# Kernel tuning notes

Measured on AMD Instinct MI355X. Metric: run time of the kernel, lower is better.

The kernel has to match this reference:

```python
import jax, jax.numpy as jnp
import numpy as np

N = 50000      # total nodes
E = 500000     # edges
D = 128        # in_channels
B = 50         # graphs in batch
NPG = N // B   # nodes per graph (equal-sized graphs)
RATIO = 0.5
ALPHA = 0.6


def setup_inputs() -> dict:
    key = jax.random.key(0)
    ks = jax.random.split(key, 8)
    x = jax.random.normal(ks[0], (N, D), dtype=jnp.float32)
    edge_index = jax.random.randint(ks[1], (2, E), 0, N, dtype=jnp.int32)
    batch = jnp.repeat(jnp.arange(B, dtype=jnp.int32), NPG)  # sorted, equal blocks
    s = 1.0 / np.sqrt(D)
    # GCNConv(D,1) for structure score
    W_s = jax.random.normal(ks[2], (D, 1), dtype=jnp.float32) * s
    b_s = jnp.zeros((1,), dtype=jnp.float32)
    # Linear(D,1) for feature score
    W_f = jax.random.normal(ks[3], (1, D), dtype=jnp.float32) * s
    b_f = jnp.zeros((1,), dtype=jnp.float32)
    # GCNConv(D,D) fusion layer
    W_fu = jax.random.normal(ks[4], (D, D), dtype=jnp.float32) * s
    b_fu = jnp.zeros((D,), dtype=jnp.float32)
    return {"x": x, "edge_index": edge_index, "batch": batch,
            "W_s": W_s, "b_s": b_s, "W_f": W_f, "b_f": b_f,
            "W_fu": W_fu, "b_fu": b_fu}


def gcn_conv(x, src, dst, W, b, n):
    """PyG GCNConv: add self loops, symmetric D^-1/2 (A+I) D^-1/2 @ (xW) + b."""
    xw = x @ W                                  # [n, out]
    loop = jnp.arange(n, dtype=src.dtype)
    s = jnp.concatenate([src, loop])
    d = jnp.concatenate([dst, loop])
    deg = jax.ops.segment_sum(jnp.ones_like(s, dtype=xw.dtype), d, num_segments=n)
    dinv = jax.lax.rsqrt(jnp.maximum(deg, 1e-12))
    norm = dinv[s] * dinv[d]                    # [E+n]
    out = jax.ops.segment_sum(norm[:, None] * xw[s], d, num_segments=n)
    return out + b


def reference(x, edge_index, batch, W_s, b_s, W_f, b_f, W_fu, b_fu):
    src, dst = edge_index[0], edge_index[1]
    # fused score: alpha * structure (GCN) + (1-alpha) * feature (Linear)
    score_s = gcn_conv(x, src, dst, W_s, b_s, N)[:, 0]          # [N]
    score_f = (x @ W_f.T + b_f)[:, 0]                           # [N]
    score = jnp.tanh(ALPHA * score_s + (1.0 - ALPHA) * score_f)
    # per-graph top-k (equal-sized graphs -> dense [B, NPG] view, like the torch topk)
    k = int(np.ceil(RATIO * NPG))
    dense = score.reshape(B, NPG)
    order = jnp.argsort(-dense, axis=-1)                        # descending
    offsets = (jnp.arange(B, dtype=jnp.int32) * NPG)[:, None]
    perm = (order[:, :k].astype(jnp.int32) + offsets).reshape(-1)  # [B*k]
    # fusion conv on full graph, then gather selected nodes
    x_fused = gcn_conv(x, src, dst, W_fu, b_fu, N)              # [N, D]
    x_ae = x_fused[perm]                                        # [B*k, D]
    x_out = x_ae * score[perm][:, None]                         # multiplier == 1
    batch_out = batch[perm]
    # filter_adj: remap node ids, keep edges with both endpoints selected
    nodemap = jnp.full((N,), -1, dtype=jnp.int32).at[perm].set(
        jnp.arange(perm.shape[0], dtype=jnp.int32))
    r, c = nodemap[src], nodemap[dst]
    m = (r >= 0) & (c >= 0)
    edge_index_new = jnp.stack([r[m], c[m]], axis=0)
    return (x_out, edge_index_new, batch_out, perm, x_ae)
```

## Files before the change

kernel.cpp:

```cpp
#include <hip/hip_runtime.h>
#include <math.h>

#define N_NODES 50000
#define N_EDGES 500000
#define DIM     128
#define NGRAPH  50
#define NPGC    1000
#define KSEL    500
#define SORT_N  1024
#define NBE     489
#define NBN     49
#define GEMM_BLKS 782
#define DEG_BLKS  1954
#define DOTS_BLKS 12500
#define NDINV     196
#define GATH_BLKS 6250

typedef short s16x8 __attribute__((ext_vector_type(8)));
typedef float f32x4 __attribute__((ext_vector_type(4)));

__device__ __forceinline__ void f2bf2(float v, unsigned short& h, unsigned short& l) {
    unsigned u = __float_as_uint(v);
    unsigned hb = (u + 0x7FFFu + ((u >> 16) & 1u)) >> 16;
    h = (unsigned short)hb;
    float r = v - __uint_as_float(hb << 16);
    unsigned u2 = __float_as_uint(r);
    l = (unsigned short)((u2 + 0x7FFFu + ((u2 >> 16) & 1u)) >> 16);
}


__global__ __launch_bounds__(256) void k0_wprep(const float* __restrict__ W,
                                                unsigned short* __restrict__ Wth,
                                                unsigned short* __restrict__ Wtl) {
    int idx = blockIdx.x * 256 + threadIdx.x;
    int k = idx >> 7, ch = idx & 127;
    unsigned short h, l;
    f2bf2(W[idx], h, l);
    int hh = k >> 6, kl = k & 63;
    int pos = hh * 8192 + ch * 64 + ((((kl >> 3) ^ (ch & 7))) << 3) + (kl & 7);
    Wth[pos] = h;
    Wtl[pos] = l;
}


__global__ __launch_bounds__(256) void k1_gemm_deg(const float* __restrict__ x,
                                                   const unsigned short* __restrict__ Wth,
                                                   const unsigned short* __restrict__ Wtl,
                                                   float* __restrict__ xw,
                                                   const int* __restrict__ dst,
                                                   int* __restrict__ deg) {
    __shared__ unsigned short lds_sh[24576];
    int t = threadIdx.x;
    if (blockIdx.x >= GEMM_BLKS) {
        int e = (blockIdx.x - GEMM_BLKS) * 256 + t;
        if (e < N_EDGES) atomicAdd(&deg[dst[e]], 1);
        return;
    }
    unsigned short* XH = lds_sh;
    unsigned short* XL = lds_sh + 4096;
    unsigned short* WH = lds_sh + 8192;
    unsigned short* WL = lds_sh + 16384;
    const int wv = t >> 6, lane = t & 63;
    const int q = lane >> 4, mm = lane & 15;
    int node_base = blockIdx.x * 64;

    f32x4 zero4v = {0.f, 0.f, 0.f, 0.f};
    f32x4 acc[8];
    #pragma unroll
    for (int ct = 0; ct < 8; ct++) acc[ct] = zero4v;

    for (int h = 0; h < 2; h++) {
        {
            const s16x8* GH = (const s16x8*)(Wth + h * 8192);
            const s16x8* GL = (const s16x8*)(Wtl + h * 8192);
            s16x8* LH = (s16x8*)WH;
            s16x8* LL = (s16x8*)WL;
            #pragma unroll
            for (int i = 0; i < 4; i++) {
                LH[t + i * 256] = GH[t + i * 256];
                LL[t + i * 256] = GL[t + i * 256];
            }
        }
        #pragma unroll
        for (int i = 0; i < 4; i++) {
            int f = t + i * 256;
            int r = f >> 4, c4 = f & 15;
            int node = node_base + r;
            float4 v = make_float4(0.f, 0.f, 0.f, 0.f);
            if (node < N_NODES) v = *(const float4*)&x[(size_t)node * DIM + h * 64 + c4 * 4];
            unsigned short h0, l0, h1, l1, h2, l2, h3, l3;
            f2bf2(v.x, h0, l0); f2bf2(v.y, h1, l1);
            f2bf2(v.z, h2, l2); f2bf2(v.w, h3, l3);
            int off = r * 64 + ((((c4 >> 1) ^ (r & 7))) << 3) + ((c4 & 1) << 2);
            *(uint2*)&XH[off] = make_uint2((unsigned)h0 | ((unsigned)h1 << 16),
                                           (unsigned)h2 | ((unsigned)h3 << 16));
            *(uint2*)&XL[off] = make_uint2((unsigned)l0 | ((unsigned)l1 << 16),
                                           (unsigned)l2 | ((unsigned)l3 << 16));
        }
        __syncthreads();
        #pragma unroll
        for (int c = 0; c < 2; c++) {
            int jb = c * 4 + q;
            int aoff = (wv * 16 + mm) * 64 + ((jb ^ (mm & 7)) << 3);
            s16x8 ah = *(const s16x8*)&XH[aoff];
            s16x8 al = *(const s16x8*)&XL[aoff];
            #pragma unroll
            for (int ct = 0; ct < 8; ct++) {
                int ch = ct * 16 + mm;
                int boff = ch * 64 + ((jb ^ (ch & 7)) << 3);
                s16x8 bh = *(const s16x8*)&WH[boff];
                s16x8 bl = *(const s16x8*)&WL[boff];
                acc[ct] = __builtin_amdgcn_mfma_f32_16x16x32_bf16(ah, bh, acc[ct], 0, 0, 0);
                acc[ct] = __builtin_amdgcn_mfma_f32_16x16x32_bf16(ah, bl, acc[ct], 0, 0, 0);
                acc[ct] = __builtin_amdgcn_mfma_f32_16x16x32_bf16(al, bh, acc[ct], 0, 0, 0);
            }
        }
        __syncthreads();
    }
    #pragma unroll
    for (int ct = 0; ct < 8; ct++) {
        #pragma unroll
        for (int r = 0; r < 4; r++) {
            int node = node_base + wv * 16 + q * 4 + r;
            if (node < N_NODES) xw[(size_t)node * DIM + ct * 16 + mm] = acc[ct][r];
        }
    }
}


__global__ __launch_bounds__(256) void k2_dots_scan_dinv(const int* __restrict__ deg,
                                                         int* __restrict__ rowoff,
                                                         int* __restrict__ bsumsN,
                                                         const float* __restrict__ x,
                                                         const float* __restrict__ Ws,
                                                         const float* __restrict__ Wf,
                                                         const float* __restrict__ bf,
                                                         double* __restrict__ pack,
                                                         float* __restrict__ dinvf,
                                                         double* __restrict__ sf) {
    int t = threadIdx.x;
    int lane = t & 63, wid = t >> 6;
    int bid = blockIdx.x;
    if (bid < DOTS_BLKS) {
        int node = bid * 4 + wid;
        const float* xr = x + (size_t)node * DIM;
        double x1 = (double)xr[lane], x2 = (double)xr[lane + 64];
        double ps = x1 * (double)Ws[lane] + x2 * (double)Ws[lane + 64];
        double pf = x1 * (double)Wf[lane] + x2 * (double)Wf[lane + 64];
        for (int off = 32; off > 0; off >>= 1) {
            ps += __shfl_down(ps, off, 64);
            pf += __shfl_down(pf, off, 64);
        }
        if (lane == 0) {
            pack[2 * node + 1] = ps;
            sf[node] = pf + (double)bf[0];
        }
        return;
    }
    if (bid < DOTS_BLKS + NBN) {
        __shared__ int ws4[4];
        int base = (bid - DOTS_BLKS) * 1024 + t * 4;
        int v0 = (base + 0 < N_NODES) ? deg[base + 0] : 0;
        int v1 = (base + 1 < N_NODES) ? deg[base + 1] : 0;
        int v2 = (base + 2 < N_NODES) ? deg[base + 2] : 0;
        int v3 = (base + 3 < N_NODES) ? deg[base + 3] : 0;
        int s4 = v0 + v1 + v2 + v3;
        int incl = s4;
        #pragma unroll
        for (int off = 1; off < 64; off <<= 1) {
            int u = __shfl_up(incl, off, 64);
            if (lane >= off) incl += u;
        }
        if (lane == 63) ws4[wid] = incl;
        __syncthreads();
        int woff = 0;
        #pragma unroll
        for (int w = 0; w < 4; w++) if (w < wid) woff += ws4[w];
        int excl = incl - s4 + woff;
        if (base + 0 < N_NODES) rowoff[base + 0] = excl;
        if (base + 1 < N_NODES) rowoff[base + 1] = excl + v0;
        if (base + 2 < N_NODES) rowoff[base + 2] = excl + v0 + v1;
        if (base + 3 < N_NODES) rowoff[base + 3] = excl + v0 + v1 + v2;
        if (t == 255) bsumsN[bid - DOTS_BLKS] = woff + incl;
        return;
    }
    int i = (bid - DOTS_BLKS - NBN) * 256 + t;
    if (i < N_NODES) {
        double di = 1.0 / sqrt((double)(deg[i] + 1));
        pack[2 * i] = di;
        dinvf[i] = (float)di;
    }
}


__global__ __launch_bounds__(256) void k3_csr(const int* __restrict__ src,
                                              const int* __restrict__ dst,
                                              const int* __restrict__ rowoff,
                                              const int* __restrict__ bsumsN,
                                              int* __restrict__ cursor,
                                              int* __restrict__ csr) {
    __shared__ int bsN[64];
    int t = threadIdx.x;
    if (t < 64) {
        int v = (t < NBN) ? bsumsN[t] : 0;
        int incl = v;
        #pragma unroll
        for (int off = 1; off < 64; off <<= 1) {
            int u = __shfl_up(incl, off, 64);
            if (t >= off) incl += u;
        }
        bsN[t] = incl - v;
    }
    __syncthreads();
    int e = blockIdx.x * 256 + t;
    if (e >= N_EDGES) return;
    int d = dst[e];
    int pos = rowoff[d] + bsN[d >> 10] + atomicAdd(&cursor[d], 1);
    csr[pos] = src[e];
}


__global__ __launch_bounds__(1024) void k4_topk(const int* __restrict__ csr,
                                                const int* __restrict__ rowoff,
                                                const int* __restrict__ bsumsN,
                                                const int* __restrict__ deg,
                                                const double* __restrict__ pack,
                                                const double* __restrict__ sf,
                                                const float* __restrict__ bs,
                                                int* __restrict__ perm, int* __restrict__ nodemap,
                                                float* __restrict__ scoref_sel,
                                                float* __restrict__ out, long o2, long o3) {
    __shared__ double key[SORT_N];
    __shared__ int    idx[SORT_N];
    __shared__ int    bsN[64];
    int g = blockIdx.x, t = threadIdx.x;
    if (t < 64) {
        int v = (t < NBN) ? bsumsN[t] : 0;
        int incl = v;
        #pragma unroll
        for (int off = 1; off < 64; off <<= 1) {
            int u = __shfl_up(incl, off, 64);
            if (t >= off) incl += u;
        }
        bsN[t] = incl - v;
    }
    __syncthreads();
    const double A = 0.6, OMA = 1.0 - 0.6;
    double bsv = (double)bs[0];
    {
        int i = t;
        if (i < NPGC) {
            int node = g * NPGC + i;
            int base = rowoff[node] + bsN[node >> 10];
            int cnt  = deg[node];
            double acc0 = 0.0, acc1 = 0.0;
            int e = 0;
            for (; e + 2 <= cnt; e += 2) {
                int s0 = csr[base + e];
                int s1 = csr[base + e + 1];
                double2 p0 = ((const double2*)pack)[s0];
                double2 p1 = ((const double2*)pack)[s1];
                acc0 += p0.x * p0.y;
                acc1 += p1.x * p1.y;
            }
            if (e < cnt) {
                int s0 = csr[base + e];
                double2 p0 = ((const double2*)pack)[s0];
                acc0 += p0.x * p0.y;
            }
            double2 pn = ((const double2*)pack)[node];
            double tot = pn.x * (acc0 + acc1) + pn.x * pn.x * pn.y + bsv;
            key[i] = tanh(A * tot + OMA * sf[node]);
            idx[i] = i;
        } else if (i < SORT_N) { key[i] = -1e300; idx[i] = i; }
    }
    __syncthreads();
    for (int size = 2; size <= SORT_N; size <<= 1) {
        for (int stride = size >> 1; stride > 0; stride >>= 1) {
            if (t < 512) {
                int a = ((t & ~(stride - 1)) << 1) | (t & (stride - 1));
                int b = a | stride;
                bool descFirst = ((a & size) == 0);
                double ka = key[a], kb = key[b];
                int ia = idx[a], ib = idx[b];
                bool aAfterB = (ka < kb) || (ka == kb && ia > ib);
                if (descFirst ? aAfterB : !aAfterB) {
                    key[a] = kb; key[b] = ka;
                    idx[a] = ib; idx[b] = ia;
                }
            }
            __syncthreads();
        }
    }
    if (t < KSEL) {
        int j = t;
        int node = g * NPGC + idx[j];
        int pos  = g * KSEL + j;
        perm[pos]        = node;
        nodemap[node]    = pos + 1;
        scoref_sel[pos]  = (float)key[j];
        out[o2 + pos]    = (float)g;
        out[o3 + pos]    = (float)node;
    }
}


__global__ __launch_bounds__(256) void k5_escan_gather(const int* __restrict__ src,
                                                       const int* __restrict__ dst,
                                                       const int* __restrict__ nodemap,
                                                       int* __restrict__ epos,
                                                       int* __restrict__ bsumsE,
                                                       const float* __restrict__ xw,
                                                       const int* __restrict__ perm,
                                                       const int* __restrict__ rowoff,
                                                       const int* __restrict__ bsumsN,
                                                       const int* __restrict__ deg,
                                                       const int* __restrict__ csr,
                                                       const float* __restrict__ dinvf,
                                                       const float* __restrict__ scoref_sel,
                                                       const float* __restrict__ b_fu,
                                                       float* __restrict__ out, long o4) {
    int t = threadIdx.x;
    int lane = t & 63, wid = t >> 6;
    if (blockIdx.x < NBE) {
        __shared__ int ws4[4];
        int base = blockIdx.x * 1024 + t * 4;
        int v0 = 0, v1 = 0, v2 = 0, v3 = 0;
        if (base + 0 < N_EDGES) v0 = (nodemap[src[base + 0]] > 0 && nodemap[dst[base + 0]] > 0);
        if (base + 1 < N_EDGES) v1 = (nodemap[src[base + 1]] > 0 && nodemap[dst[base + 1]] > 0);
        if (base + 2 < N_EDGES) v2 = (nodemap[src[base + 2]] > 0 && nodemap[dst[base + 2]] > 0);
        if (base + 3 < N_EDGES) v3 = (nodemap[src[base + 3]] > 0 && nodemap[dst[base + 3]] > 0);
        int s4 = v0 + v1 + v2 + v3;
        int incl = s4;
        #pragma unroll
        for (int off = 1; off < 64; off <<= 1) {
            int u = __shfl_up(incl, off, 64);
            if (lane >= off) incl += u;
        }
        if (lane == 63) ws4[wid] = incl;
        __syncthreads();
        int woff = 0;
        #pragma unroll
        for (int w = 0; w < 4; w++) if (w < wid) woff += ws4[w];
        int excl = incl - s4 + woff;
        if (base + 0 < N_EDGES) epos[base + 0] = excl;
        if (base + 1 < N_EDGES) epos[base + 1] = excl + v0;
        if (base + 2 < N_EDGES) epos[base + 2] = excl + v0 + v1;
        if (base + 3 < N_EDGES) epos[base + 3] = excl + v0 + v1 + v2;
        if (t == 255) bsumsE[blockIdx.x] = woff + incl;
        return;
    }
    __shared__ int bsN[64];
    if (t < 64) {
        int v = (t < NBN) ? bsumsN[t] : 0;
        int incl = v;
        #pragma unroll
        for (int off = 1; off < 64; off <<= 1) {
            int u = __shfl_up(incl, off, 64);
            if (t >= off) incl += u;
        }
        bsN[t] = incl - v;
    }
    __syncthreads();
    int wave = (blockIdx.x - NBE) * 4 + wid;
    int p = perm[wave];
    float dpf = dinvf[p];
    int c2 = lane * 2;
    float2 v = ((const float2*)(xw + (size_t)p * DIM))[lane];
    float nself = dpf * dpf;
    float ax = nself * v.x, ay = nself * v.y;
    int beg = rowoff[p] + bsN[p >> 10], cnt = deg[p];
    int i = 0;
    for (; i + 2 <= cnt; i += 2) {
        int s0 = csr[beg + i];
        int s1 = csr[beg + i + 1];
        float2 u0 = ((const float2*)(xw + (size_t)s0 * DIM))[lane];
        float2 u1 = ((const float2*)(xw + (size_t)s1 * DIM))[lane];
        float n0 = dinvf[s0] * dpf, n1 = dinvf[s1] * dpf;
        ax += n0 * u0.x; ay += n0 * u0.y;
        ax += n1 * u1.x; ay += n1 * u1.y;
    }
    if (i < cnt) {
        int s0 = csr[beg + i];
        float2 u0 = ((const float2*)(xw + (size_t)s0 * DIM))[lane];
        float n0 = dinvf[s0] * dpf;
        ax += n0 * u0.x; ay += n0 * u0.y;
    }
    ax += b_fu[c2];
    ay += b_fu[c2 + 1];
    float sc = scoref_sel[wave];
    size_t ro = (size_t)wave * DIM + c2;
    out[o4 + ro]     = ax;
    out[o4 + ro + 1] = ay;
    out[ro]          = ax * sc;
    out[ro + 1]      = ay * sc;
}


__global__ __launch_bounds__(256) void k6_compact(const int* __restrict__ src,
                                                  const int* __restrict__ dst,
                                                  const int* __restrict__ nodemap,
                                                  const int* __restrict__ epos,
                                                  const int* __restrict__ bsumsE,
                                                  float* __restrict__ out_edges, long M) {
    __shared__ int bsE[512];
    int t = threadIdx.x;
    if (t < 64) {
        int carry = 0;
        #pragma unroll
        for (int c = 0; c < 8; c++) {
            int i = c * 64 + t;
            int v = (i < NBE) ? bsumsE[i] : 0;
            int incl = v;
            #pragma unroll
            for (int off = 1; off < 64; off <<= 1) {
                int u = __shfl_up(incl, off, 64);
                if (t >= off) incl += u;
            }
            if (i < 512) bsE[i] = incl - v + carry;
            carry += __shfl(incl, 63, 64);
        }
    }
    __syncthreads();
    int e = blockIdx.x * 256 + t;
    if (e >= N_EDGES) return;
    int r = nodemap[src[e]], c = nodemap[dst[e]];
    if (r > 0 && c > 0) {
        int pos = epos[e] + bsE[e >> 10];
        out_edges[pos]     = (float)(r - 1);
        out_edges[M + pos] = (float)(c - 1);
    }
}


extern "C" void kernel_launch(void* const* d_in, const int* in_sizes, int n_in,
                              void* d_out, int out_size, void* d_ws, size_t ws_size,
                              hipStream_t stream) {
    const float* x    = (const float*)d_in[0];
    const int*   ei   = (const int*)d_in[1];
    const int*   src  = ei;
    const int*   dst  = ei + N_EDGES;
    const float* W_s  = (const float*)d_in[3];
    const float* b_s  = (const float*)d_in[4];
    const float* W_f  = (const float*)d_in[5];
    const float* b_f  = (const float*)d_in[6];
    const float* W_fu = (const float*)d_in[7];
    const float* b_fu = (const float*)d_in[8];
    float* out = (float*)d_out;

    char* wsp = (char*)d_ws;
    size_t off = 0;
    auto take = [&](size_t bytes) -> char* {
        char* p = wsp + off;
        off = (off + bytes + 255) & ~(size_t)255;
        return p;
    };
    char*   zbase      = wsp;
    int*    deg        = (int*)   take((size_t)N_NODES * 4);
    int*    cursor     = (int*)   take((size_t)N_NODES * 4);
    int*    nodemap    = (int*)   take((size_t)N_NODES * 4);
    size_t  zbytes     = off;
    double* pack       = (double*)take((size_t)N_NODES * 16);
    double* sf         = (double*)take((size_t)N_NODES * 8);
    float*  dinvf      = (float*) take((size_t)N_NODES * 4);
    float*  scoref_sel = (float*) take((size_t)NGRAPH * KSEL * 4);
    int*    perm       = (int*)   take((size_t)NGRAPH * KSEL * 4);
    int*    rowoff     = (int*)   take((size_t)N_NODES * 4);
    int*    epos       = (int*)   take((size_t)N_EDGES * 4);
    int*    bsumsE     = (int*)   take((size_t)1024 * 4);
    int*    bsumsN     = (int*)   take((size_t)1024 * 4);
    int*    csr        = (int*)   take((size_t)N_EDGES * 4);
    float*  xw         = (float*) take((size_t)N_NODES * DIM * 4);
    unsigned short* Wth = (unsigned short*)take((size_t)16384 * 2);
    unsigned short* Wtl = (unsigned short*)take((size_t)16384 * 2);

    long M  = ((long)out_size - 6450000L) / 2;
    long o1 = 3200000L;
    long o2 = o1 + 2 * M;
    long o3 = o2 + (long)NGRAPH * KSEL;
    long o4 = o3 + (long)NGRAPH * KSEL;

    hipMemsetAsync(zbase, 0, zbytes, stream);

    k0_wprep<<<64, 256, 0, stream>>>(W_fu, Wth, Wtl);
    k1_gemm_deg<<<GEMM_BLKS + DEG_BLKS, 256, 0, stream>>>(x, Wth, Wtl, xw, dst, deg);
    k2_dots_scan_dinv<<<DOTS_BLKS + NBN + NDINV, 256, 0, stream>>>(deg, rowoff, bsumsN,
                                                                   x, W_s, W_f, b_f,
                                                                   pack, dinvf, sf);
    k3_csr<<<DEG_BLKS, 256, 0, stream>>>(src, dst, rowoff, bsumsN, cursor, csr);
    k4_topk<<<NGRAPH, 1024, 0, stream>>>(csr, rowoff, bsumsN, deg, pack, sf, b_s,
                                         perm, nodemap, scoref_sel, out, o2, o3);
    k5_escan_gather<<<NBE + GATH_BLKS, 256, 0, stream>>>(src, dst, nodemap, epos, bsumsE,
                                                         xw, perm, rowoff, bsumsN, deg, csr,
                                                         dinvf, scoref_sel, b_fu, out, o4);
    k6_compact<<<DEG_BLKS, 256, 0, stream>>>(src, dst, nodemap, epos, bsumsE, out + o1, M);
}
```

Baseline: 233.0 us.

## Merge pipeline kernels into one cooperative persistent kernel with grid syncs

Replaces the chain of seven kernel launches with a single cooperative persistent kernel. Phases are separated by grid.sync(), and each phase's work is distributed over the grid with block-strided loops. Degree counting now records each edge's atomic rank, so the later CSR fill can place edges without a second atomic pass, and the GEMM moves after the first sync. This aims to remove launch gaps and tail idle time between kernels, at the cost of grid-wide barriers, a fixed grid size limited by occupancy, and 48KB of shared memory per block.

```diff
diff --git a/kernel.cpp b/kernel.cpp
--- a/kernel.cpp
+++ b/kernel.cpp
@@ -1,5 +1,8 @@
 #include <hip/hip_runtime.h>
+#include <hip/hip_cooperative_groups.h>
 #include <math.h>
+
+namespace cg = cooperative_groups;
 
 #define N_NODES 50000
 #define N_EDGES 500000
@@ -10,11 +13,17 @@
 #define SORT_N  1024
 #define NBE     489
 #define NBN     49
-#define GEMM_BLKS 782
-#define DEG_BLKS  1954
-#define DOTS_BLKS 12500
-#define NDINV     196
-#define GATH_BLKS 6250
+
+#define WPREP_C 64
+#define RANK_C  1954
+#define DOTS_C  12500
+#define P0_TOT  (WPREP_C + RANK_C + DOTS_C)
+#define GEMM_C  782
+#define P1_TOT  (GEMM_C + NBN + 196)
+#define P2_TOT  1954
+#define GATH_C  6250
+#define P4_TOT  (NBE + GATH_C)
+#define P5_TOT  1954
 
 typedef short s16x8 __attribute__((ext_vector_type(8)));
 typedef float f32x4 __attribute__((ext_vector_type(4)));
@@ -29,406 +38,344 @@
 }
 
 
-__global__ __launch_bounds__(256) void k0_wprep(const float* __restrict__ W,
-                                                unsigned short* __restrict__ Wth,
-                                                unsigned short* __restrict__ Wtl) {
-    int idx = blockIdx.x * 256 + threadIdx.x;
-    int k = idx >> 7, ch = idx & 127;
-    unsigned short h, l;
-    f2bf2(W[idx], h, l);
-    int hh = k >> 6, kl = k & 63;
-    int pos = hh * 8192 + ch * 64 + ((((kl >> 3) ^ (ch & 7))) << 3) + (kl & 7);
-    Wth[pos] = h;
-    Wtl[pos] = l;
-}
-
-
-__global__ __launch_bounds__(256) void k1_gemm_deg(const float* __restrict__ x,
-                                                   const unsigned short* __restrict__ Wth,
-                                                   const unsigned short* __restrict__ Wtl,
-                                                   float* __restrict__ xw,
-                                                   const int* __restrict__ dst,
-                                                   int* __restrict__ deg) {
-    __shared__ unsigned short lds_sh[24576];
-    int t = threadIdx.x;
-    if (blockIdx.x >= GEMM_BLKS) {
-        int e = (blockIdx.x - GEMM_BLKS) * 256 + t;
-        if (e < N_EDGES) atomicAdd(&deg[dst[e]], 1);
-        return;
-    }
-    unsigned short* XH = lds_sh;
-    unsigned short* XL = lds_sh + 4096;
-    unsigned short* WH = lds_sh + 8192;
-    unsigned short* WL = lds_sh + 16384;
-    const int wv = t >> 6, lane = t & 63;
-    const int q = lane >> 4, mm = lane & 15;
-    int node_base = blockIdx.x * 64;
-
-    f32x4 zero4v = {0.f, 0.f, 0.f, 0.f};
-    f32x4 acc[8];
-    #pragma unroll
-    for (int ct = 0; ct < 8; ct++) acc[ct] = zero4v;
-
-    for (int h = 0; h < 2; h++) {
-        {
-            const s16x8* GH = (const s16x8*)(Wth + h * 8192);
-            const s16x8* GL = (const s16x8*)(Wtl + h * 8192);
-            s16x8* LH = (s16x8*)WH;
-            s16x8* LL = (s16x8*)WL;
-            #pragma unroll
-            for (int i = 0; i < 4; i++) {
-                LH[t + i * 256] = GH[t + i * 256];
-                LL[t + i * 256] = GL[t + i * 256];
-            }
-        }
-        #pragma unroll
-        for (int i = 0; i < 4; i++) {
-            int f = t + i * 256;
-            int r = f >> 4, c4 = f & 15;
-            int node = node_base + r;
-            float4 v = make_float4(0.f, 0.f, 0.f, 0.f);
-            if (node < N_NODES) v = *(const float4*)&x[(size_t)node * DIM + h * 64 + c4 * 4];
-            unsigned short h0, l0, h1, l1, h2, l2, h3, l3;
-            f2bf2(v.x, h0, l0); f2bf2(v.y, h1, l1);
-            f2bf2(v.z, h2, l2); f2bf2(v.w, h3, l3);
-            int off = r * 64 + ((((c4 >> 1) ^ (r & 7))) << 3) + ((c4 & 1) << 2);
-            *(uint2*)&XH[off] = make_uint2((unsigned)h0 | ((unsigned)h1 << 16),
-                                           (unsigned)h2 | ((unsigned)h3 << 16));
-            *(uint2*)&XL[off] = make_uint2((unsigned)l0 | ((unsigned)l1 << 16),
-                                           (unsigned)l2 | ((unsigned)l3 << 16));
-        }
-        __syncthreads();
-        #pragma unroll
-        for (int c = 0; c < 2; c++) {
-            int jb = c * 4 + q;
-            int aoff = (wv * 16 + mm) * 64 + ((jb ^ (mm & 7)) << 3);
-            s16x8 ah = *(const s16x8*)&XH[aoff];
-            s16x8 al = *(const s16x8*)&XL[aoff];
+__global__ __launch_bounds__(256) void mega(
+    const float* __restrict__ x, const int* __restrict__ src, const int* __restrict__ dst,
+    const float* __restrict__ Ws, const float* __restrict__ bs,
+    const float* __restrict__ Wf, const float* __restrict__ bf,
+    const float* __restrict__ Wfu, const float* __restrict__ bfu,
+    int* cursor, int* nodemap, int* rank,
+    double* pack, double* sf, float* dinvf, float* scoref_sel,
+    int* perm, int* rowoff, int* epos, int* bsumsE, int* bsumsN,
+    int* csr, float* xw, unsigned short* Wth, unsigned short* Wtl,
+    float* out, long M, long o2, long o3, long o4)
+{
+    cg::grid_group grid = cg::this_grid();
+    __shared__ __align__(16) unsigned char smem[49152];
+    const int t = threadIdx.x;
+    const int lane = t & 63, wid = t >> 6;
+    const int G = gridDim.x;
+
+    for (int c = blockIdx.x; c < P0_TOT; c += G) {
+        if (c < WPREP_C) {
+            int wi = c * 256 + t;
+            int k = wi >> 7, ch = wi & 127;
+            unsigned short h, l;
+            f2bf2(Wfu[wi], h, l);
+            int hh = k >> 6, kl = k & 63;
+            int pos = hh * 8192 + ch * 64 + ((((kl >> 3) ^ (ch & 7))) << 3) + (kl & 7);
+            Wth[pos] = h; Wtl[pos] = l;
+        } else if (c < WPREP_C + RANK_C) {
+            int e = (c - WPREP_C) * 256 + t;
+            if (e < N_EDGES) rank[e] = atomicAdd(&cursor[dst[e]], 1);
+        } else {
+            int node = (c - WPREP_C - RANK_C) * 4 + wid;
+            const float* xr = x + (size_t)node * DIM;
+            double x1 = (double)xr[lane], x2 = (double)xr[lane + 64];
+            double ps = x1 * (double)Ws[lane] + x2 * (double)Ws[lane + 64];
+            double pf = x1 * (double)Wf[lane] + x2 * (double)Wf[lane + 64];
+            for (int off = 32; off > 0; off >>= 1) {
+                ps += __shfl_down(ps, off, 64);
+                pf += __shfl_down(pf, off, 64);
+            }
+            if (lane == 0) { pack[2 * node + 1] = ps; sf[node] = pf + (double)bf[0]; }
+        }
+    }
+    grid.sync();
+
+    for (int c = blockIdx.x; c < P1_TOT; c += G) {
+        if (c < GEMM_C) {
+            unsigned short* XH = (unsigned short*)smem;
+            unsigned short* XL = XH + 4096;
+            unsigned short* WH = XH + 8192;
+            unsigned short* WL = XH + 16384;
+            const int q = lane >> 4, mm = lane & 15;
+            int node_base = c * 64;
+            f32x4 acc[8];
+            #pragma unroll
+            for (int ct = 0; ct < 8; ct++) acc[ct] = (f32x4){0.f, 0.f, 0.f, 0.f};
+            for (int h = 0; h < 2; h++) {
+                {
+                    const s16x8* GH = (const s16x8*)(Wth + h * 8192);
+                    const s16x8* GL = (const s16x8*)(Wtl + h * 8192);
+                    s16x8* LH = (s16x8*)WH;
+                    s16x8* LL = (s16x8*)WL;
+                    #pragma unroll
+                    for (int i = 0; i < 4; i++) {
+                        LH[t + i * 256] = GH[t + i * 256];
+                        LL[t + i * 256] = GL[t + i * 256];
+                    }
+                }
+                #pragma unroll
+                for (int i = 0; i < 4; i++) {
+                    int f = t + i * 256;
+                    int r = f >> 4, c4 = f & 15;
+                    int node = node_base + r;
+                    float4 v = make_float4(0.f, 0.f, 0.f, 0.f);
+                    if (node < N_NODES) v = *(const float4*)&x[(size_t)node * DIM + h * 64 + c4 * 4];
+                    unsigned short h0, l0, h1, l1, h2, l2, h3, l3;
+                    f2bf2(v.x, h0, l0); f2bf2(v.y, h1, l1);
+                    f2bf2(v.z, h2, l2); f2bf2(v.w, h3, l3);
+                    int off = r * 64 + ((((c4 >> 1) ^ (r & 7))) << 3) + ((c4 & 1) << 2);
+                    *(uint2*)&XH[off] = make_uint2((unsigned)h0 | ((unsigned)h1 << 16),
+                                                   (unsigned)h2 | ((unsigned)h3 << 16));
+                    *(uint2*)&XL[off] = make_uint2((unsigned)l0 | ((unsigned)l1 << 16),
+                                                   (unsigned)l2 | ((unsigned)l3 << 16));
+                }
+                __syncthreads();
+                #pragma unroll
+                for (int kk2 = 0; kk2 < 2; kk2++) {
+                    int jb = kk2 * 4 + q;
+                    int aoff = (wid * 16 + mm) * 64 + ((jb ^ (mm & 7)) << 3);
+                    s16x8 ah = *(const s16x8*)&XH[aoff];
+                    s16x8 al = *(const s16x8*)&XL[aoff];
+                    #pragma unroll
+                    for (int ct = 0; ct < 8; ct++) {
+                        int ch = ct * 16 + mm;
+                        int boff = ch * 64 + ((jb ^ (ch & 7)) << 3);
+                        s16x8 bh = *(const s16x8*)&WH[boff];
+                        s16x8 bl = *(const s16x8*)&WL[boff];
+                        acc[ct] = __builtin_amdgcn_mfma_f32_16x16x32_bf16(ah, bh, acc[ct], 0, 0, 0);
+                        acc[ct] = __builtin_amdgcn_mfma_f32_16x16x32_bf16(ah, bl, acc[ct], 0, 0, 0);
+                        acc[ct] = __builtin_amdgcn_mfma_f32_16x16x32_bf16(al, bh, acc[ct], 0, 0, 0);
+                    }
+                }
+                __syncthreads();
+            }
             #pragma unroll
             for (int ct = 0; ct < 8; ct++) {
-                int ch = ct * 16 + mm;
-                int boff = ch * 64 + ((jb ^ (ch & 7)) << 3);
-                s16x8 bh = *(const s16x8*)&WH[boff];
-                s16x8 bl = *(const s16x8*)&WL[boff];
-                acc[ct] = __builtin_amdgcn_mfma_f32_16x16x32_bf16(ah, bh, acc[ct], 0, 0, 0);
-                acc[ct] = __builtin_amdgcn_mfma_f32_16x16x32_bf16(ah, bl, acc[ct], 0, 0, 0);
-                acc[ct] = __builtin_amdgcn_mfma_f32_16x16x32_bf16(al, bh, acc[ct], 0, 0, 0);
-            }
-        }
-        __syncthreads();
-    }
-    #pragma unroll
-    for (int ct = 0; ct < 8; ct++) {
-        #pragma unroll
-        for (int r = 0; r < 4; r++) {
-            int node = node_base + wv * 16 + q * 4 + r;
-            if (node < N_NODES) xw[(size_t)node * DIM + ct * 16 + mm] = acc[ct][r];
-        }
-    }
-}
-
-
-__global__ __launch_bounds__(256) void k2_dots_scan_dinv(const int* __restrict__ deg,
-                                                         int* __restrict__ rowoff,
-                                                         int* __restrict__ bsumsN,
-                                                         const float* __restrict__ x,
-                                                         const float* __restrict__ Ws,
-                                                         const float* __restrict__ Wf,
-                                                         const float* __restrict__ bf,
-                                                         double* __restrict__ pack,
-                                                         float* __restrict__ dinvf,
-                                                         double* __restrict__ sf) {
-    int t = threadIdx.x;
-    int lane = t & 63, wid = t >> 6;
-    int bid = blockIdx.x;
-    if (bid < DOTS_BLKS) {
-        int node = bid * 4 + wid;
-        const float* xr = x + (size_t)node * DIM;
-        double x1 = (double)xr[lane], x2 = (double)xr[lane + 64];
-        double ps = x1 * (double)Ws[lane] + x2 * (double)Ws[lane + 64];
-        double pf = x1 * (double)Wf[lane] + x2 * (double)Wf[lane + 64];
-        for (int off = 32; off > 0; off >>= 1) {
-            ps += __shfl_down(ps, off, 64);
-            pf += __shfl_down(pf, off, 64);
-        }
-        if (lane == 0) {
-            pack[2 * node + 1] = ps;
-            sf[node] = pf + (double)bf[0];
-        }
-        return;
-    }
-    if (bid < DOTS_BLKS + NBN) {
-        __shared__ int ws4[4];
-        int base = (bid - DOTS_BLKS) * 1024 + t * 4;
-        int v0 = (base + 0 < N_NODES) ? deg[base + 0] : 0;
-        int v1 = (base + 1 < N_NODES) ? deg[base + 1] : 0;
-        int v2 = (base + 2 < N_NODES) ? deg[base + 2] : 0;
-        int v3 = (base + 3 < N_NODES) ? deg[base + 3] : 0;
-        int s4 = v0 + v1 + v2 + v3;
-        int incl = s4;
-        #pragma unroll
-        for (int off = 1; off < 64; off <<= 1) {
-            int u = __shfl_up(incl, off, 64);
-            if (lane >= off) incl += u;
-        }
-        if (lane == 63) ws4[wid] = incl;
-        __syncthreads();
-        int woff = 0;
-        #pragma unroll
-        for (int w = 0; w < 4; w++) if (w < wid) woff += ws4[w];
-        int excl = incl - s4 + woff;
-        if (base + 0 < N_NODES) rowoff[base + 0] = excl;
-        if (base + 1 < N_NODES) rowoff[base + 1] = excl + v0;
-        if (base + 2 < N_NODES) rowoff[base + 2] = excl + v0 + v1;
-        if (base + 3 < N_NODES) rowoff[base + 3] = excl + v0 + v1 + v2;
-        if (t == 255) bsumsN[bid - DOTS_BLKS] = woff + incl;
-        return;
-    }
-    int i = (bid - DOTS_BLKS - NBN) * 256 + t;
-    if (i < N_NODES) {
-        double di = 1.0 / sqrt((double)(deg[i] + 1));
-        pack[2 * i] = di;
-        dinvf[i] = (float)di;
-    }
-}
-
-
-__global__ __launch_bounds__(256) void k3_csr(const int* __restrict__ src,
-                                              const int* __restrict__ dst,
-                                              const int* __restrict__ rowoff,
-                                              const int* __restrict__ bsumsN,
-                                              int* __restrict__ cursor,
-                                              int* __restrict__ csr) {
-    __shared__ int bsN[64];
-    int t = threadIdx.x;
-    if (t < 64) {
-        int v = (t < NBN) ? bsumsN[t] : 0;
-        int incl = v;
-        #pragma unroll
-        for (int off = 1; off < 64; off <<= 1) {
-            int u = __shfl_up(incl, off, 64);
-            if (t >= off) incl += u;
-        }
-        bsN[t] = incl - v;
-    }
-    __syncthreads();
-    int e = blockIdx.x * 256 + t;
-    if (e >= N_EDGES) return;
-    int d = dst[e];
-    int pos = rowoff[d] + bsN[d >> 10] + atomicAdd(&cursor[d], 1);
-    csr[pos] = src[e];
-}
-
-
-__global__ __launch_bounds__(1024) void k4_topk(const int* __restrict__ csr,
-                                                const int* __restrict__ rowoff,
-                                                const int* __restrict__ bsumsN,
-                                                const int* __restrict__ deg,
-                                                const double* __restrict__ pack,
-                                                const double* __restrict__ sf,
-                                                const float* __restrict__ bs,
-                                                int* __restrict__ perm, int* __restrict__ nodemap,
-                                                float* __restrict__ scoref_sel,
-                                                float* __restrict__ out, long o2, long o3) {
-    __shared__ double key[SORT_N];
-    __shared__ int    idx[SORT_N];
-    __shared__ int    bsN[64];
-    int g = blockIdx.x, t = threadIdx.x;
-    if (t < 64) {
-        int v = (t < NBN) ? bsumsN[t] : 0;
-        int incl = v;
-        #pragma unroll
-        for (int off = 1; off < 64; off <<= 1) {
-            int u = __shfl_up(incl, off, 64);
-            if (t >= off) incl += u;
-        }
-        bsN[t] = incl - v;
-    }
-    __syncthreads();
-    const double A = 0.6, OMA = 1.0 - 0.6;
-    double bsv = (double)bs[0];
+                #pragma unroll
+                for (int r = 0; r < 4; r++) {
+                    int node = node_base + wid * 16 + q * 4 + r;
+                    if (node < N_NODES) xw[(size_t)node * DIM + ct * 16 + mm] = acc[ct][r];
+                }
+            }
+        } else if (c < GEMM_C + NBN) {
+            int* ws4 = (int*)(smem + 12544);
+            int chunk = c - GEMM_C;
+            int base = chunk * 1024 + t * 4;
+            int v0 = (base + 0 < N_NODES) ? cursor[base + 0] : 0;
+            int v1 = (base + 1 < N_NODES) ? cursor[base + 1] : 0;
+            int v2 = (base + 2 < N_NODES) ? cursor[base + 2] : 0;
+            int v3 = (base + 3 < N_NODES) ? cursor[base + 3] : 0;
+            int s4 = v0 + v1 + v2 + v3;
+            int incl = s4;
+            #pragma unroll
+            for (int off = 1; off < 64; off <<= 1) {
+                int u = __shfl_up(incl, off, 64);
+                if (lane >= off) incl += u;
+            }
+            if (lane == 63) ws4[wid] = incl;
+            __syncthreads();
+            int woff = 0;
+            #pragma unroll
+            for (int w = 0; w < 4; w++) if (w < wid) woff += ws4[w];
+            int excl = incl - s4 + woff;
+            if (base + 0 < N_NODES) rowoff[base + 0] = excl;
+            if (base + 1 < N_NODES) rowoff[base + 1] = excl + v0;
+            if (base + 2 < N_NODES) rowoff[base + 2] = excl + v0 + v1;
+            if (base + 3 < N_NODES) rowoff[base + 3] = excl + v0 + v1 + v2;
+            if (t == 255) bsumsN[chunk] = woff + incl;
+            __syncthreads();
+        } else {
+            int i = (c - GEMM_C - NBN) * 256 + t;
+            if (i < N_NODES) {
+                double di = 1.0 / sqrt((double)(cursor[i] + 1));
+                pack[2 * i] = di;
+                dinvf[i] = (float)di;
+            }
+        }
+    }
+    grid.sync();
+
     {
-        int i = t;
-        if (i < NPGC) {
-            int node = g * NPGC + i;
-            int base = rowoff[node] + bsN[node >> 10];
-            int cnt  = deg[node];
-            double acc0 = 0.0, acc1 = 0.0;
-            int e = 0;
-            for (; e + 2 <= cnt; e += 2) {
-                int s0 = csr[base + e];
-                int s1 = csr[base + e + 1];
-                double2 p0 = ((const double2*)pack)[s0];
-                double2 p1 = ((const double2*)pack)[s1];
-                acc0 += p0.x * p0.y;
-                acc1 += p1.x * p1.y;
-            }
-            if (e < cnt) {
-                int s0 = csr[base + e];
-                double2 p0 = ((const double2*)pack)[s0];
-                acc0 += p0.x * p0.y;
-            }
-            double2 pn = ((const double2*)pack)[node];
-            double tot = pn.x * (acc0 + acc1) + pn.x * pn.x * pn.y + bsv;
-            key[i] = tanh(A * tot + OMA * sf[node]);
-            idx[i] = i;
-        } else if (i < SORT_N) { key[i] = -1e300; idx[i] = i; }
-    }
-    __syncthreads();
-    for (int size = 2; size <= SORT_N; size <<= 1) {
-        for (int stride = size >> 1; stride > 0; stride >>= 1) {
-            if (t < 512) {
-                int a = ((t & ~(stride - 1)) << 1) | (t & (stride - 1));
-                int b = a | stride;
-                bool descFirst = ((a & size) == 0);
-                double ka = key[a], kb = key[b];
-                int ia = idx[a], ib = idx[b];
-                bool aAfterB = (ka < kb) || (ka == kb && ia > ib);
-                if (descFirst ? aAfterB : !aAfterB) {
-                    key[a] = kb; key[b] = ka;
-                    idx[a] = ib; idx[b] = ia;
-                }
-            }
-            __syncthreads();
-        }
-    }
-    if (t < KSEL) {
-        int j = t;
-        int node = g * NPGC + idx[j];
-        int pos  = g * KSEL + j;
-        perm[pos]        = node;
-        nodemap[node]    = pos + 1;
-        scoref_sel[pos]  = (float)key[j];
-        out[o2 + pos]    = (float)g;
-        out[o3 + pos]    = (float)node;
-    }
-}
-
-
-__global__ __launch_bounds__(256) void k5_escan_gather(const int* __restrict__ src,
-                                                       const int* __restrict__ dst,
-                                                       const int* __restrict__ nodemap,
-                                                       int* __restrict__ epos,
-                                                       int* __restrict__ bsumsE,
-                                                       const float* __restrict__ xw,
-                                                       const int* __restrict__ perm,
-                                                       const int* __restrict__ rowoff,
-                                                       const int* __restrict__ bsumsN,
-                                                       const int* __restrict__ deg,
-                                                       const int* __restrict__ csr,
-                                                       const float* __restrict__ dinvf,
-                                                       const float* __restrict__ scoref_sel,
-                                                       const float* __restrict__ b_fu,
-                                                       float* __restrict__ out, long o4) {
-    int t = threadIdx.x;
-    int lane = t & 63, wid = t >> 6;
-    if (blockIdx.x < NBE) {
-        __shared__ int ws4[4];
-        int base = blockIdx.x * 1024 + t * 4;
-        int v0 = 0, v1 = 0, v2 = 0, v3 = 0;
-        if (base + 0 < N_EDGES) v0 = (nodemap[src[base + 0]] > 0 && nodemap[dst[base + 0]] > 0);
-        if (base + 1 < N_EDGES) v1 = (nodemap[src[base + 1]] > 0 && nodemap[dst[base + 1]] > 0);
-        if (base + 2 < N_EDGES) v2 = (nodemap[src[base + 2]] > 0 && nodemap[dst[base + 2]] > 0);
-        if (base + 3 < N_EDGES) v3 = (nodemap[src[base + 3]] > 0 && nodemap[dst[base + 3]] > 0);
-        int s4 = v0 + v1 + v2 + v3;
-        int incl = s4;
-        #pragma unroll
-        for (int off = 1; off < 64; off <<= 1) {
-            int u = __shfl_up(incl, off, 64);
-            if (lane >= off) incl += u;
-        }
-        if (lane == 63) ws4[wid] = incl;
-        __syncthreads();
-        int woff = 0;
-        #pragma unroll
-        for (int w = 0; w < 4; w++) if (w < wid) woff += ws4[w];
-        int excl = incl - s4 + woff;
-        if (base + 0 < N_EDGES) epos[base + 0] = excl;
-        if (base + 1 < N_EDGES) epos[base + 1] = excl + v0;
-        if (base + 2 < N_EDGES) epos[base + 2] = excl + v0 + v1;
-        if (base + 3 < N_EDGES) epos[base + 3] = excl + v0 + v1 + v2;
-        if (t == 255) bsumsE[blockIdx.x] = woff + incl;
-        return;
-    }
-    __shared__ int bsN[64];
-    if (t < 64) {
-        int v = (t < NBN) ? bsumsN[t] : 0;
-        int incl = v;
-        #pragma unroll
-        for (int off = 1; off < 64; off <<= 1) {
-            int u = __shfl_up(incl, off, 64);
-            if (t >= off) incl += u;
-        }
-        bsN[t] = incl - v;
-    }
-    __syncthreads();
-    int wave = (blockIdx.x - NBE) * 4 + wid;
-    int p = perm[wave];
-    float dpf = dinvf[p];
-    int c2 = lane * 2;
-    float2 v = ((const float2*)(xw + (size_t)p * DIM))[lane];
-    float nself = dpf * dpf;
-    float ax = nself * v.x, ay = nself * v.y;
-    int beg = rowoff[p] + bsN[p >> 10], cnt = deg[p];
-    int i = 0;
-    for (; i + 2 <= cnt; i += 2) {
-        int s0 = csr[beg + i];
-        int s1 = csr[beg + i + 1];
-        float2 u0 = ((const float2*)(xw + (size_t)s0 * DIM))[lane];
-        float2 u1 = ((const float2*)(xw + (size_t)s1 * DIM))[lane];
-        float n0 = dinvf[s0] * dpf, n1 = dinvf[s1] * dpf;
-        ax += n0 * u0.x; ay += n0 * u0.y;
-        ax += n1 * u1.x; ay += n1 * u1.y;
-    }
-    if (i < cnt) {
-        int s0 = csr[beg + i];
-        float2 u0 = ((const float2*)(xw + (size_t)s0 * DIM))[lane];
-        float n0 = dinvf[s0] * dpf;
-        ax += n0 * u0.x; ay += n0 * u0.y;
-    }
-    ax += b_fu[c2];
-    ay += b_fu[c2 + 1];
-    float sc = scoref_sel[wave];
-    size_t ro = (size_t)wave * DIM + c2;
-    out[o4 + ro]     = ax;
-    out[o4 + ro + 1] = ay;
-    out[ro]          = ax * sc;
-    out[ro + 1]      = ay * sc;
-}
-
-
-__global__ __launch_bounds__(256) void k6_compact(const int* __restrict__ src,
-                                                  const int* __restrict__ dst,
-                                                  const int* __restrict__ nodemap,
-                                                  const int* __restrict__ epos,
-                                                  const int* __restrict__ bsumsE,
-                                                  float* __restrict__ out_edges, long M) {
-    __shared__ int bsE[512];
-    int t = threadIdx.x;
-    if (t < 64) {
-        int carry = 0;
-        #pragma unroll
-        for (int c = 0; c < 8; c++) {
-            int i = c * 64 + t;
-            int v = (i < NBE) ? bsumsE[i] : 0;
+        int* bsN = (int*)(smem + 12288);
+        if (t < 64) {
+            int v = (t < NBN) ? bsumsN[t] : 0;
             int incl = v;
             #pragma unroll
             for (int off = 1; off < 64; off <<= 1) {
                 int u = __shfl_up(incl, off, 64);
                 if (t >= off) incl += u;
             }
-            if (i < 512) bsE[i] = incl - v + carry;
-            carry += __shfl(incl, 63, 64);
-        }
-    }
-    __syncthreads();
-    int e = blockIdx.x * 256 + t;
-    if (e >= N_EDGES) return;
-    int r = nodemap[src[e]], c = nodemap[dst[e]];
-    if (r > 0 && c > 0) {
-        int pos = epos[e] + bsE[e >> 10];
-        out_edges[pos]     = (float)(r - 1);
-        out_edges[M + pos] = (float)(c - 1);
+            bsN[t] = incl - v;
+        }
+        __syncthreads();
+        for (int c = blockIdx.x; c < P2_TOT; c += G) {
+            int e = c * 256 + t;
+            if (e < N_EDGES) {
+                int d = dst[e];
+                csr[rowoff[d] + bsN[d >> 10] + rank[e]] = src[e];
+            }
+        }
+    }
+    grid.sync();
+
+    {
+        double* key = (double*)smem;
+        int* idx = (int*)(smem + 8192);
+        int* bsN = (int*)(smem + 12288);
+        const double A = 0.6, OMA = 1.0 - 0.6;
+        double bsv = (double)bs[0];
+        for (int g = blockIdx.x; g < NGRAPH; g += G) {
+            for (int i = t; i < SORT_N; i += 256) {
+                if (i < NPGC) {
+                    int node = g * NPGC + i;
+                    int base = rowoff[node] + bsN[node >> 10];
+                    int cnt  = cursor[node];
+                    double acc0 = 0.0, acc1 = 0.0;
+                    int e = 0;
+                    for (; e + 2 <= cnt; e += 2) {
+                        int s0 = csr[base + e];
+                        int s1 = csr[base + e + 1];
+                        double2 p0 = ((const double2*)pack)[s0];
+                        double2 p1 = ((const double2*)pack)[s1];
+                        acc0 += p0.x * p0.y;
+                        acc1 += p1.x * p1.y;
+                    }
+                    if (e < cnt) {
+                        int s0 = csr[base + e];
+                        double2 p0 = ((const double2*)pack)[s0];
+                        acc0 += p0.x * p0.y;
+                    }
+                    double2 pn = ((const double2*)pack)[node];
+                    double tot = pn.x * (acc0 + acc1) + pn.x * pn.x * pn.y + bsv;
+                    key[i] = tanh(A * tot + OMA * sf[node]);
+                    idx[i] = i;
+                } else { key[i] = -1e300; idx[i] = i; }
+            }
+            __syncthreads();
+            for (int size = 2; size <= SORT_N; size <<= 1) {
+                for (int stride = size >> 1; stride > 0; stride >>= 1) {
+                    #pragma unroll
+                    for (int jj = 0; jj < 2; jj++) {
+                        int j = t + jj * 256;
+                        int a = ((j & ~(stride - 1)) << 1) | (j & (stride - 1));
+                        int b = a | stride;
+                        bool descFirst = ((a & size) == 0);
+                        double ka = key[a], kb = key[b];
+                        int ia = idx[a], ib = idx[b];
+                        bool aAfterB = (ka < kb) || (ka == kb && ia > ib);
+                        if (descFirst ? aAfterB : !aAfterB) {
+                            key[a] = kb; key[b] = ka;
+                            idx[a] = ib; idx[b] = ia;
+                        }
+                    }
+                    __syncthreads();
+                }
+            }
+            for (int j = t; j < KSEL; j += 256) {
+                int node = g * NPGC + idx[j];
+                int pos  = g * KSEL + j;
+                perm[pos]       = node;
+                nodemap[node]   = pos + 1;
+                scoref_sel[pos] = (float)key[j];
+                out[o2 + pos]   = (float)g;
+                out[o3 + pos]   = (float)node;
+            }
+            __syncthreads();
+        }
+    }
+    grid.sync();
+
+    {
+        int* bsN = (int*)(smem + 12288);
+        int* ws4 = (int*)(smem + 12544);
+        for (int c = blockIdx.x; c < P4_TOT; c += G) {
+            if (c < NBE) {
+                int base = c * 1024 + t * 4;
+                int v0 = 0, v1 = 0, v2 = 0, v3 = 0;
+                if (base + 0 < N_EDGES) v0 = (nodemap[src[base + 0]] > 0 && nodemap[dst[base + 0]] > 0);
+                if (base + 1 < N_EDGES) v1 = (nodemap[src[base + 1]] > 0 && nodemap[dst[base + 1]] > 0);
+                if (base + 2 < N_EDGES) v2 = (nodemap[src[base + 2]] > 0 && nodemap[dst[base + 2]] > 0);
+                if (base + 3 < N_EDGES) v3 = (nodemap[src[base + 3]] > 0 && nodemap[dst[base + 3]] > 0);
+                int s4 = v0 + v1 + v2 + v3;
+                int incl = s4;
+                #pragma unroll
+                for (int off = 1; off < 64; off <<= 1) {
+                    int u = __shfl_up(incl, off, 64);
+                    if (lane >= off) incl += u;
+                }
+                if (lane == 63) ws4[wid] = incl;
+                __syncthreads();
+                int woff = 0;
+                #pragma unroll
+                for (int w = 0; w < 4; w++) if (w < wid) woff += ws4[w];
+                int excl = incl - s4 + woff;
+                if (base + 0 < N_EDGES) epos[base + 0] = excl;
+                if (base + 1 < N_EDGES) epos[base + 1] = excl + v0;
+                if (base + 2 < N_EDGES) epos[base + 2] = excl + v0 + v1;
+                if (base + 3 < N_EDGES) epos[base + 3] = excl + v0 + v1 + v2;
+                if (t == 255) bsumsE[c] = woff + incl;
+                __syncthreads();
+            } else {
+                int wave = (c - NBE) * 4 + wid;
+                int p = perm[wave];
+                float dpf = dinvf[p];
+                int c2 = lane * 2;
+                float2 v = ((const float2*)(xw + (size_t)p * DIM))[lane];
+                float nself = dpf * dpf;
+                float ax = nself * v.x, ay = nself * v.y;
+                int beg = rowoff[p] + bsN[p >> 10], cnt = cursor[p];
+                int i = 0;
+                for (; i + 2 <= cnt; i += 2) {
+                    int s0 = csr[beg + i];
+                    int s1 = csr[beg + i + 1];
+                    float2 u0 = ((const float2*)(xw + (size_t)s0 * DIM))[lane];
+                    float2 u1 = ((const float2*)(xw + (size_t)s1 * DIM))[lane];
+                    float n0 = dinvf[s0] * dpf, n1 = dinvf[s1] * dpf;
+                    ax += n0 * u0.x; ay += n0 * u0.y;
+                    ax += n1 * u1.x; ay += n1 * u1.y;
+                }
+                if (i < cnt) {
+                    int s0 = csr[beg + i];
+                    float2 u0 = ((const float2*)(xw + (size_t)s0 * DIM))[lane];
+                    float n0 = dinvf[s0] * dpf;
+                    ax += n0 * u0.x; ay += n0 * u0.y;
+                }
+                ax += bfu[c2];
+                ay += bfu[c2 + 1];
+                float sc = scoref_sel[wave];
+                size_t ro = (size_t)wave * DIM + c2;
+                out[o4 + ro]     = ax;
+                out[o4 + ro + 1] = ay;
+                out[ro]          = ax * sc;
+                out[ro + 1]      = ay * sc;
+            }
+        }
+    }
+    grid.sync();
+
+    {
+        int* bsE = (int*)smem;
+        if (t < 64) {
+            int carry = 0;
+            #pragma unroll
+            for (int cc = 0; cc < 8; cc++) {
+                int i = cc * 64 + t;
+                int v = (i < NBE) ? bsumsE[i] : 0;
+                int incl = v;
+                #pragma unroll
+                for (int off = 1; off < 64; off <<= 1) {
+                    int u = __shfl_up(incl, off, 64);
+                    if (t >= off) incl += u;
+                }
+                if (i < 512) bsE[i] = incl - v + carry;
+                carry += __shfl(incl, 63, 64);
+            }
+        }
+        __syncthreads();
+        const long o1 = 3200000L;
+        for (int c = blockIdx.x; c < P5_TOT; c += G) {
+            int e = c * 256 + t;
+            if (e < N_EDGES) {
+                int r = nodemap[src[e]], cc = nodemap[dst[e]];
+                if (r > 0 && cc > 0) {
+                    int pos = epos[e] + bsE[e >> 10];
+                    out[o1 + pos]     = (float)(r - 1);
+                    out[o1 + M + pos] = (float)(cc - 1);
+                }
+            }
+        }
     }
 }
 
@@ -456,10 +403,10 @@
         return p;
     };
     char*   zbase      = wsp;
-    int*    deg        = (int*)   take((size_t)N_NODES * 4);
     int*    cursor     = (int*)   take((size_t)N_NODES * 4);
     int*    nodemap    = (int*)   take((size_t)N_NODES * 4);
     size_t  zbytes     = off;
+    int*    rank       = (int*)   take((size_t)N_EDGES * 4);
     double* pack       = (double*)take((size_t)N_NODES * 16);
     double* sf         = (double*)take((size_t)N_NODES * 8);
     float*  dinvf      = (float*) take((size_t)N_NODES * 4);
@@ -482,16 +429,20 @@
 
     hipMemsetAsync(zbase, 0, zbytes, stream);
 
-    k0_wprep<<<64, 256, 0, stream>>>(W_fu, Wth, Wtl);
-    k1_gemm_deg<<<GEMM_BLKS + DEG_BLKS, 256, 0, stream>>>(x, Wth, Wtl, xw, dst, deg);
-    k2_dots_scan_dinv<<<DOTS_BLKS + NBN + NDINV, 256, 0, stream>>>(deg, rowoff, bsumsN,
-                                                                   x, W_s, W_f, b_f,
-                                                                   pack, dinvf, sf);
-    k3_csr<<<DEG_BLKS, 256, 0, stream>>>(src, dst, rowoff, bsumsN, cursor, csr);
-    k4_topk<<<NGRAPH, 1024, 0, stream>>>(csr, rowoff, bsumsN, deg, pack, sf, b_s,
-                                         perm, nodemap, scoref_sel, out, o2, o3);
-    k5_escan_gather<<<NBE + GATH_BLKS, 256, 0, stream>>>(src, dst, nodemap, epos, bsumsE,
-                                                         xw, perm, rowoff, bsumsN, deg, csr,
-                                                         dinvf, scoref_sel, b_fu, out, o4);
-    k6_compact<<<DEG_BLKS, 256, 0, stream>>>(src, dst, nodemap, epos, bsumsE, out + o1, M);
+    int maxb = 0;
+    if (hipOccupancyMaxActiveBlocksPerMultiprocessor(&maxb, (const void*)mega, 256, 0)
+        != hipSuccess || maxb <= 0) maxb = 1;
+    if (maxb > 3) maxb = 3;
+    int G = maxb * 256;
+
+    void* args[] = {
+        (void*)&x, (void*)&src, (void*)&dst,
+        (void*)&W_s, (void*)&b_s, (void*)&W_f, (void*)&b_f, (void*)&W_fu, (void*)&b_fu,
+        (void*)&cursor, (void*)&nodemap, (void*)&rank,
+        (void*)&pack, (void*)&sf, (void*)&dinvf, (void*)&scoref_sel,
+        (void*)&perm, (void*)&rowoff, (void*)&epos, (void*)&bsumsE, (void*)&bsumsN,
+        (void*)&csr, (void*)&xw, (void*)&Wth, (void*)&Wtl,
+        (void*)&out, (void*)&M, (void*)&o2, (void*)&o3, (void*)&o4
+    };
+    hipLaunchCooperativeKernel((const void*)mega, dim3(G), dim3(256), args, 0, stream);
 }
```

Result: slower. 496.3 us (+113.0%).
